# Performance work log

Hardware: AMD Instinct MI355X
Metric: run time of the kernel (lower is better)

The kernel has to match this reference:

```python
import jax, jax.numpy as jnp
import numpy as np

N, DEG, F = 500000, 16, 128
H1, H2, OUT = 256, 256, 128


def setup_inputs() -> dict:
    key = jax.random.key(0)
    ks = jax.random.split(key, 8)
    s = lambda fan_in: 1.0 / np.sqrt(fan_in)
    return {
        "message": jax.random.normal(ks[0], (N, DEG, F), dtype=jnp.float32),
        "features": jax.random.normal(ks[1], (N, F), dtype=jnp.float32),
        "global_features": jax.random.normal(ks[2], (N, F), dtype=jnp.float32),
        "W1": jax.random.normal(ks[3], (3 * F, H1), dtype=jnp.float32) * s(3 * F),
        "b1": jnp.zeros((H1,), dtype=jnp.float32),
        "W2": jax.random.normal(ks[4], (H1, H2), dtype=jnp.float32) * s(H1),
        "b2": jnp.zeros((H2,), dtype=jnp.float32),
        "W3": jax.random.normal(ks[5], (H2, OUT), dtype=jnp.float32) * s(H2),
        "b3": jnp.zeros((OUT,), dtype=jnp.float32),
    }


def reference(message, features, global_features, W1, b1, W2, b2, W3, b3):
    # mailbox sum-aggregate over neighbors: [N, deg, F] -> [N, F]
    agg = jnp.sum(message, axis=1)
    # concat aggregated messages with node + global features: [N, 3F]
    x = jnp.concatenate([agg, features, global_features], axis=1)
    # MLP: Linear+ReLU, Linear+ReLU, Linear
    h = jax.nn.relu(x @ W1 + b1)
    h = jax.nn.relu(h @ W2 + b2)
    out = h @ W3 + b3
    # row-wise L2 (Frobenius over dim=1) normalization
    norm = jnp.linalg.norm(out, axis=1, keepdims=True)
    return out / (norm + 1e-8)
```

## Files before the change

### kernel.cpp

```cpp
#include <hip/hip_runtime.h>


typedef short short8   __attribute__((ext_vector_type(8)));
typedef short short4_t __attribute__((ext_vector_type(4)));
typedef float f32x4    __attribute__((ext_vector_type(4)));

#define SWZ(row, off) ((off) ^ (((row) & 7) << 4))

__device__ __forceinline__ unsigned short f2bf(float f) {
    unsigned int u = __float_as_uint(f);
    u += 0x7fffu + ((u >> 16) & 1u);
    return (unsigned short)(u >> 16);
}

__global__ void prep_weights(const float* __restrict__ W1,
                             const float* __restrict__ W2,
                             const float* __restrict__ W3,
                             short* __restrict__ pw1,
                             short* __restrict__ pw2,
                             short* __restrict__ pw3) {
    int idx = blockIdx.x * 256 + threadIdx.x;
    if (idx < 98304) {
        int j = idx & 7, l = (idx >> 3) & 63, g = idx >> 9;
        int ks = g % 12, tn = g / 12;
        int n = tn * 16 + (l & 15);
        int k = ks * 32 + ((l >> 4) << 3) + j;
        pw1[idx] = (short)f2bf(W1[k * 256 + n]);
    } else if (idx < 98304 + 65536) {
        int e = idx - 98304;
        int j = e & 7, l = (e >> 3) & 63, g = e >> 9;
        int ks = g & 7, tn = g >> 3;
        int n = tn * 16 + (l & 15);
        int k = ks * 32 + ((l >> 4) << 3) + j;
        pw2[e] = (short)f2bf(W2[k * 256 + n]);
    } else if (idx < 98304 + 65536 + 32768) {
        int e = idx - 98304 - 65536;
        int j = e & 7, l = (e >> 3) & 63, g = e >> 9;
        int ks = g & 7, tn = g >> 3;
        int n = tn * 16 + (l & 15);
        int k = ks * 32 + ((l >> 4) << 3) + j;
        pw3[e] = (short)f2bf(W3[k * 128 + n]);
    }
}

__global__ __launch_bounds__(256, 4) void node_net_fused(
    const float* __restrict__ msg,
    const float* __restrict__ feat,
    const float* __restrict__ glob,
    const float* __restrict__ b1v,
    const float* __restrict__ b2v,
    const float* __restrict__ b3v,
    const short* __restrict__ pw1,
    const short* __restrict__ pw2,
    const short* __restrict__ pw3,
    float* __restrict__ out,
    int n_rows)
{
    __shared__ char lds[32768];
    char* regA = lds;
    char* regB = lds + 16384;

    const int tid  = threadIdx.x;
    const int lane = tid & 63;
    const int w    = tid >> 6;
    const int lr   = lane & 15;
    const int lk   = lane >> 4;
    const long long r0 = (long long)blockIdx.x * 32;

    const f32x4 zero4 = {0.f, 0.f, 0.f, 0.f};

    f32x4 fr[4], gr[4];
    #pragma unroll
    for (int q = 0; q < 4; ++q) {
        int r = (tid >> 5) + q * 8;
        long long row = r0 + r;
        fr[q] = zero4; gr[q] = zero4;
        if (row < n_rows) {
            fr[q] = __builtin_nontemporal_load((const f32x4*)feat + row * 32 + (tid & 31));
            gr[q] = __builtin_nontemporal_load((const f32x4*)glob + row * 32 + (tid & 31));
        }
    }

    #pragma unroll 1
    for (int pp = 0; pp < 4; ++pp) {
        const int rA = 8 * w + 2 * pp;
        const long long rowA = r0 + rA;
        const f32x4* base = (const f32x4*)msg + rowA * 512;
        f32x4 tA[8], tB[8];
        const bool okA = rowA < n_rows;
        const bool okB = (rowA + 1) < n_rows;
        if (okA) {
            #pragma unroll
            for (int i = 0; i < 8; ++i) tA[i] = __builtin_nontemporal_load(base + i * 64 + lane);
        } else {
            #pragma unroll
            for (int i = 0; i < 8; ++i) tA[i] = zero4;
        }
        if (okB) {
            #pragma unroll
            for (int i = 0; i < 8; ++i) tB[i] = __builtin_nontemporal_load(base + 512 + i * 64 + lane);
        } else {
            #pragma unroll
            for (int i = 0; i < 8; ++i) tB[i] = zero4;
        }
        f32x4 sA = ((tA[0] + tA[1]) + (tA[2] + tA[3])) + ((tA[4] + tA[5]) + (tA[6] + tA[7]));
        f32x4 sB = ((tB[0] + tB[1]) + (tB[2] + tB[3])) + ((tB[4] + tB[5]) + (tB[6] + tB[7]));
        #pragma unroll
        for (int c = 0; c < 4; ++c) {
            sA[c] += __shfl_xor(sA[c], 32);
            sB[c] += __shfl_xor(sB[c], 32);
        }
        f32x4 s = (lane < 32) ? sA : sB;
        short4_t s4;
        s4[0] = (short)f2bf(s[0]); s4[1] = (short)f2bf(s[1]);
        s4[2] = (short)f2bf(s[2]); s4[3] = (short)f2bf(s[3]);
        const int orow = rA + (lane >> 5);
        *(short4_t*)(regB + SWZ(orow, orow * 256 + (lane & 31) * 8)) = s4;
    }
    __syncthreads();

    #pragma unroll
    for (int q = 0; q < 4; ++q) {
        int r = (tid >> 5) + q * 8;
        short4_t s4;
        s4[0] = (short)f2bf(fr[q][0]); s4[1] = (short)f2bf(fr[q][1]);
        s4[2] = (short)f2bf(fr[q][2]); s4[3] = (short)f2bf(fr[q][3]);
        *(short4_t*)(regA + SWZ(r, r * 256 + (tid & 31) * 8)) = s4;
    }

    f32x4 acc1[2][4];
    #pragma unroll
    for (int ri = 0; ri < 2; ++ri)
        #pragma unroll
        for (int ci = 0; ci < 4; ++ci) acc1[ri][ci] = zero4;

    #pragma unroll
    for (int s = 0; s < 4; ++s) {
        short8 a[2], b[4];
        #pragma unroll
        for (int ri = 0; ri < 2; ++ri) {
            int row = ri * 16 + lr;
            a[ri] = *(const short8*)(regB + SWZ(row, row * 256 + s * 64 + lk * 16));
        }
        #pragma unroll
        for (int ci = 0; ci < 4; ++ci) {
            int tn = w * 4 + ci;
            b[ci] = *(const short8*)(pw1 + (((tn * 12 + s) * 64 + lane) << 3));
        }
        #pragma unroll
        for (int ri = 0; ri < 2; ++ri)
            #pragma unroll
            for (int ci = 0; ci < 4; ++ci)
                acc1[ri][ci] = __builtin_amdgcn_mfma_f32_16x16x32_bf16(
                    a[ri], b[ci], acc1[ri][ci], 0, 0, 0);
    }
    __syncthreads();

    #pragma unroll
    for (int q = 0; q < 4; ++q) {
        int r = (tid >> 5) + q * 8;
        short4_t s4;
        s4[0] = (short)f2bf(gr[q][0]); s4[1] = (short)f2bf(gr[q][1]);
        s4[2] = (short)f2bf(gr[q][2]); s4[3] = (short)f2bf(gr[q][3]);
        *(short4_t*)(regB + 8192 + SWZ(r, r * 256 + (tid & 31) * 8)) = s4;
    }

    #pragma unroll
    for (int s = 0; s < 4; ++s) {
        short8 a[2], b[4];
        #pragma unroll
        for (int ri = 0; ri < 2; ++ri) {
            int row = ri * 16 + lr;
            a[ri] = *(const short8*)(regA + SWZ(row, row * 256 + s * 64 + lk * 16));
        }
        #pragma unroll
        for (int ci = 0; ci < 4; ++ci) {
            int tn = w * 4 + ci;
            b[ci] = *(const short8*)(pw1 + (((tn * 12 + 4 + s) * 64 + lane) << 3));
        }
        #pragma unroll
        for (int ri = 0; ri < 2; ++ri)
            #pragma unroll
            for (int ci = 0; ci < 4; ++ci)
                acc1[ri][ci] = __builtin_amdgcn_mfma_f32_16x16x32_bf16(
                    a[ri], b[ci], acc1[ri][ci], 0, 0, 0);
    }
    __syncthreads();

    #pragma unroll
    for (int s = 0; s < 4; ++s) {
        short8 a[2], b[4];
        #pragma unroll
        for (int ri = 0; ri < 2; ++ri) {
            int row = ri * 16 + lr;
            a[ri] = *(const short8*)(regB + 8192 + SWZ(row, row * 256 + s * 64 + lk * 16));
        }
        #pragma unroll
        for (int ci = 0; ci < 4; ++ci) {
            int tn = w * 4 + ci;
            b[ci] = *(const short8*)(pw1 + (((tn * 12 + 8 + s) * 64 + lane) << 3));
        }
        #pragma unroll
        for (int ri = 0; ri < 2; ++ri)
            #pragma unroll
            for (int ci = 0; ci < 4; ++ci)
                acc1[ri][ci] = __builtin_amdgcn_mfma_f32_16x16x32_bf16(
                    a[ri], b[ci], acc1[ri][ci], 0, 0, 0);
    }

    #pragma unroll
    for (int ci = 0; ci < 4; ++ci) {
        int col = w * 64 + ci * 16 + lr;
        float bias = b1v[col];
        #pragma unroll
        for (int ri = 0; ri < 2; ++ri)
            #pragma unroll
            for (int i = 0; i < 4; ++i) {
                int row = ri * 16 + lk * 4 + i;
                float v = fmaxf(acc1[ri][ci][i] + bias, 0.f);
                *(short*)(regA + SWZ(row, row * 512 + col * 2)) = (short)f2bf(v);
            }
    }
    __syncthreads();

    f32x4 acc2[2][4];
    #pragma unroll
    for (int ri = 0; ri < 2; ++ri)
        #pragma unroll
        for (int ci = 0; ci < 4; ++ci) acc2[ri][ci] = zero4;

    #pragma unroll
    for (int s = 0; s < 8; ++s) {
        short8 a[2], b[4];
        #pragma unroll
        for (int ri = 0; ri < 2; ++ri) {
            int row = ri * 16 + lr;
            a[ri] = *(const short8*)(regA + SWZ(row, row * 512 + s * 64 + lk * 16));
        }
        #pragma unroll
        for (int ci = 0; ci < 4; ++ci) {
            int tn = w * 4 + ci;
            b[ci] = *(const short8*)(pw2 + (((tn * 8 + s) * 64 + lane) << 3));
        }
        #pragma unroll
        for (int ri = 0; ri < 2; ++ri)
            #pragma unroll
            for (int ci = 0; ci < 4; ++ci)
                acc2[ri][ci] = __builtin_amdgcn_mfma_f32_16x16x32_bf16(
                    a[ri], b[ci], acc2[ri][ci], 0, 0, 0);
    }

    #pragma unroll
    for (int ci = 0; ci < 4; ++ci) {
        int col = w * 64 + ci * 16 + lr;
        float bias = b2v[col];
        #pragma unroll
        for (int ri = 0; ri < 2; ++ri)
            #pragma unroll
            for (int i = 0; i < 4; ++i) {
                int row = ri * 16 + lk * 4 + i;
                float v = fmaxf(acc2[ri][ci][i] + bias, 0.f);
                *(short*)(regB + SWZ(row, row * 512 + col * 2)) = (short)f2bf(v);
            }
    }
    __syncthreads();

    f32x4 acc3[2][2];
    #pragma unroll
    for (int ri = 0; ri < 2; ++ri)
        #pragma unroll
        for (int ci = 0; ci < 2; ++ci) acc3[ri][ci] = zero4;

    #pragma unroll
    for (int s = 0; s < 8; ++s) {
        short8 a[2], b[2];
        #pragma unroll
        for (int ri = 0; ri < 2; ++ri) {
            int row = ri * 16 + lr;
            a[ri] = *(const short8*)(regB + SWZ(row, row * 512 + s * 64 + lk * 16));
        }
        #pragma unroll
        for (int ci = 0; ci < 2; ++ci) {
            int tn = w * 2 + ci;
            b[ci] = *(const short8*)(pw3 + (((tn * 8 + s) * 64 + lane) << 3));
        }
        #pragma unroll
        for (int ri = 0; ri < 2; ++ri)
            #pragma unroll
            for (int ci = 0; ci < 2; ++ci)
                acc3[ri][ci] = __builtin_amdgcn_mfma_f32_16x16x32_bf16(
                    a[ri], b[ci], acc3[ri][ci], 0, 0, 0);
    }

    #pragma unroll
    for (int ci = 0; ci < 2; ++ci) {
        int col = w * 32 + ci * 16 + lr;
        float bias = b3v[col];
        #pragma unroll
        for (int ri = 0; ri < 2; ++ri)
            #pragma unroll
            for (int i = 0; i < 4; ++i) {
                int row = ri * 16 + lk * 4 + i;
                float v = acc3[ri][ci][i] + bias;
                *(float*)(regA + SWZ(row, row * 512 + col * 4)) = v;
            }
    }
    __syncthreads();

    #pragma unroll
    for (int pass = 0; pass < 4; ++pass) {
        const int r  = (tid >> 5) + pass * 8;
        const int fl = tid & 31;
        f32x4 v = *(const f32x4*)(regA + SWZ(r, r * 512 + fl * 16));
        float ss = v[0]*v[0] + v[1]*v[1] + v[2]*v[2] + v[3]*v[3];
        ss += __shfl_xor(ss, 1, 32);
        ss += __shfl_xor(ss, 2, 32);
        ss += __shfl_xor(ss, 4, 32);
        ss += __shfl_xor(ss, 8, 32);
        ss += __shfl_xor(ss, 16, 32);
        float inv = 1.f / (sqrtf(ss) + 1e-8f);
        long long row = r0 + r;
        if (row < n_rows) {
            f32x4 o = v * inv;
            __builtin_nontemporal_store(o, (f32x4*)out + row * 32 + fl);
        }
    }
}

extern "C" void kernel_launch(void* const* d_in, const int* in_sizes, int n_in,
                              void* d_out, int out_size, void* d_ws, size_t ws_size,
                              hipStream_t stream) {
    const float* msg  = (const float*)d_in[0];
    const float* feat = (const float*)d_in[1];
    const float* glob = (const float*)d_in[2];
    const float* W1   = (const float*)d_in[3];
    const float* b1   = (const float*)d_in[4];
    const float* W2   = (const float*)d_in[5];
    const float* b2   = (const float*)d_in[6];
    const float* W3   = (const float*)d_in[7];
    const float* b3   = (const float*)d_in[8];
    float* out = (float*)d_out;

    const int n_rows = in_sizes[1] / 128;

    short* pw1 = (short*)d_ws;
    short* pw2 = pw1 + 98304;
    short* pw3 = pw2 + 65536;

    hipLaunchKernelGGL(prep_weights, dim3(768), dim3(256), 0, stream,
                       W1, W2, W3, pw1, pw2, pw3);

    const int nblocks = (n_rows + 31) / 32;
    hipLaunchKernelGGL(node_net_fused, dim3(nblocks), dim3(256), 0, stream,
                       msg, feat, glob, b1, b2, b3, pw1, pw2, pw3, out, n_rows);
}
```

Measured before the change: 1.080 ms.

## Convert fused node MLP to persistent blocks with software-pipelined message prefetch

The one-block-per-tile launch becomes a persistent grid of at most 1024 blocks that loop over 32-row tiles. While the MFMA layers run for the current tile, each block loads the next tile's message rows, features and global features, so the memory stream overlaps with compute. Biases are hoisted into registers, and features and globals are staged in a larger LDS buffer. The cost is more LDS per block (40KB), more register pressure from the in-flight prefetch registers, and fewer blocks in flight to hide latency.

```diff
diff --git a/kernel.cpp b/kernel.cpp
--- a/kernel.cpp
+++ b/kernel.cpp
@@ -43,7 +43,36 @@
     }
 }
 
-__global__ __launch_bounds__(256, 4) void node_net_fused(
+#define ISSUE(j) {                                                            \
+    const long long rowg_ = rn0 + 8 * w + (j);                                \
+    if (rowg_ < n_rows) {                                                     \
+        const f32x4* bp_ = (const f32x4*)msg + rowg_ * 512 + lane;            \
+        T[0] = __builtin_nontemporal_load(bp_ + 0 * 64);                      \
+        T[1] = __builtin_nontemporal_load(bp_ + 1 * 64);                      \
+        T[2] = __builtin_nontemporal_load(bp_ + 2 * 64);                      \
+        T[3] = __builtin_nontemporal_load(bp_ + 3 * 64);                      \
+        T[4] = __builtin_nontemporal_load(bp_ + 4 * 64);                      \
+        T[5] = __builtin_nontemporal_load(bp_ + 5 * 64);                      \
+        T[6] = __builtin_nontemporal_load(bp_ + 6 * 64);                      \
+        T[7] = __builtin_nontemporal_load(bp_ + 7 * 64);                      \
+    } else {                                                                  \
+        T[0]=zero4; T[1]=zero4; T[2]=zero4; T[3]=zero4;                       \
+        T[4]=zero4; T[5]=zero4; T[6]=zero4; T[7]=zero4;                       \
+    } }
+
+#define CONSUME(j) {                                                          \
+    f32x4 s_ = ((T[0]+T[1])+(T[2]+T[3])) + ((T[4]+T[5])+(T[6]+T[7]));         \
+    s_[0] += __shfl_xor(s_[0], 32); s_[1] += __shfl_xor(s_[1], 32);           \
+    s_[2] += __shfl_xor(s_[2], 32); s_[3] += __shfl_xor(s_[3], 32);           \
+    if (lane < 32) {                                                          \
+        short4_t s4_;                                                         \
+        s4_[0]=(short)f2bf(s_[0]); s4_[1]=(short)f2bf(s_[1]);                 \
+        s4_[2]=(short)f2bf(s_[2]); s4_[3]=(short)f2bf(s_[3]);                 \
+        const int rj_ = 8 * w + (j);                                          \
+        *(short4_t*)(XB + SWZ(rj_, rj_ * 256 + (lane & 31) * 8)) = s4_;       \
+    } }
+
+__global__ __launch_bounds__(256, 4) void node_net_pipe(
     const float* __restrict__ msg,
     const float* __restrict__ feat,
     const float* __restrict__ glob,
@@ -54,275 +83,281 @@
     const short* __restrict__ pw2,
     const short* __restrict__ pw3,
     float* __restrict__ out,
-    int n_rows)
+    int n_rows, int ntiles, int nblk)
 {
-    __shared__ char lds[32768];
-    char* regA = lds;
-    char* regB = lds + 16384;
+    __shared__ char lds[40960];
+    char* XB = lds;
+    char* HB = lds + 24576;
 
     const int tid  = threadIdx.x;
     const int lane = tid & 63;
     const int w    = tid >> 6;
     const int lr   = lane & 15;
     const int lk   = lane >> 4;
-    const long long r0 = (long long)blockIdx.x * 32;
-
     const f32x4 zero4 = {0.f, 0.f, 0.f, 0.f};
 
-    f32x4 fr[4], gr[4];
+    float bias1[4], bias2[4], bias3[2];
     #pragma unroll
-    for (int q = 0; q < 4; ++q) {
-        int r = (tid >> 5) + q * 8;
-        long long row = r0 + r;
-        fr[q] = zero4; gr[q] = zero4;
-        if (row < n_rows) {
-            fr[q] = __builtin_nontemporal_load((const f32x4*)feat + row * 32 + (tid & 31));
-            gr[q] = __builtin_nontemporal_load((const f32x4*)glob + row * 32 + (tid & 31));
-        }
+    for (int ci = 0; ci < 4; ++ci) {
+        bias1[ci] = b1v[w * 64 + ci * 16 + lr];
+        bias2[ci] = b2v[w * 64 + ci * 16 + lr];
     }
-
-    #pragma unroll 1
-    for (int pp = 0; pp < 4; ++pp) {
-        const int rA = 8 * w + 2 * pp;
-        const long long rowA = r0 + rA;
-        const f32x4* base = (const f32x4*)msg + rowA * 512;
-        f32x4 tA[8], tB[8];
-        const bool okA = rowA < n_rows;
-        const bool okB = (rowA + 1) < n_rows;
-        if (okA) {
-            #pragma unroll
-            for (int i = 0; i < 8; ++i) tA[i] = __builtin_nontemporal_load(base + i * 64 + lane);
-        } else {
-            #pragma unroll
-            for (int i = 0; i < 8; ++i) tA[i] = zero4;
-        }
-        if (okB) {
-            #pragma unroll
-            for (int i = 0; i < 8; ++i) tB[i] = __builtin_nontemporal_load(base + 512 + i * 64 + lane);
-        } else {
-            #pragma unroll
-            for (int i = 0; i < 8; ++i) tB[i] = zero4;
-        }
-        f32x4 sA = ((tA[0] + tA[1]) + (tA[2] + tA[3])) + ((tA[4] + tA[5]) + (tA[6] + tA[7]));
-        f32x4 sB = ((tB[0] + tB[1]) + (tB[2] + tB[3])) + ((tB[4] + tB[5]) + (tB[6] + tB[7]));
-        #pragma unroll
-        for (int c = 0; c < 4; ++c) {
-            sA[c] += __shfl_xor(sA[c], 32);
-            sB[c] += __shfl_xor(sB[c], 32);
-        }
-        f32x4 s = (lane < 32) ? sA : sB;
-        short4_t s4;
-        s4[0] = (short)f2bf(s[0]); s4[1] = (short)f2bf(s[1]);
-        s4[2] = (short)f2bf(s[2]); s4[3] = (short)f2bf(s[3]);
-        const int orow = rA + (lane >> 5);
-        *(short4_t*)(regB + SWZ(orow, orow * 256 + (lane & 31) * 8)) = s4;
+    #pragma unroll
+    for (int ci = 0; ci < 2; ++ci) bias3[ci] = b3v[w * 32 + ci * 16 + lr];
+
+    long long t = blockIdx.x;
+
+    {
+        const long long r0 = t * 32;
+        f32x4 fr[4], gr[4];
+        #pragma unroll
+        for (int q = 0; q < 4; ++q) {
+            int r = (tid >> 5) + q * 8;
+            long long row = r0 + r;
+            fr[q] = zero4; gr[q] = zero4;
+            if (row < n_rows) {
+                fr[q] = __builtin_nontemporal_load((const f32x4*)feat + row * 32 + (tid & 31));
+                gr[q] = __builtin_nontemporal_load((const f32x4*)glob + row * 32 + (tid & 31));
+            }
+        }
+        #pragma unroll 1
+        for (int pp = 0; pp < 4; ++pp) {
+            const int rA = 8 * w + 2 * pp;
+            const long long rowA = r0 + rA;
+            const f32x4* base = (const f32x4*)msg + rowA * 512;
+            f32x4 tA[8], tB[8];
+            const bool okA = rowA < n_rows;
+            const bool okB = (rowA + 1) < n_rows;
+            #pragma unroll
+            for (int i = 0; i < 8; ++i)
+                tA[i] = okA ? __builtin_nontemporal_load(base + i * 64 + lane) : zero4;
+            #pragma unroll
+            for (int i = 0; i < 8; ++i)
+                tB[i] = okB ? __builtin_nontemporal_load(base + 512 + i * 64 + lane) : zero4;
+            f32x4 sA = ((tA[0]+tA[1])+(tA[2]+tA[3])) + ((tA[4]+tA[5])+(tA[6]+tA[7]));
+            f32x4 sB = ((tB[0]+tB[1])+(tB[2]+tB[3])) + ((tB[4]+tB[5])+(tB[6]+tB[7]));
+            #pragma unroll
+            for (int c = 0; c < 4; ++c) {
+                sA[c] += __shfl_xor(sA[c], 32);
+                sB[c] += __shfl_xor(sB[c], 32);
+            }
+            f32x4 s = (lane < 32) ? sA : sB;
+            short4_t s4;
+            s4[0]=(short)f2bf(s[0]); s4[1]=(short)f2bf(s[1]);
+            s4[2]=(short)f2bf(s[2]); s4[3]=(short)f2bf(s[3]);
+            const int orow = rA + (lane >> 5);
+            *(short4_t*)(XB + SWZ(orow, orow * 256 + (lane & 31) * 8)) = s4;
+        }
+        #pragma unroll
+        for (int q = 0; q < 4; ++q) {
+            int r = (tid >> 5) + q * 8;
+            short4_t sf, sg;
+            sf[0]=(short)f2bf(fr[q][0]); sf[1]=(short)f2bf(fr[q][1]);
+            sf[2]=(short)f2bf(fr[q][2]); sf[3]=(short)f2bf(fr[q][3]);
+            sg[0]=(short)f2bf(gr[q][0]); sg[1]=(short)f2bf(gr[q][1]);
+            sg[2]=(short)f2bf(gr[q][2]); sg[3]=(short)f2bf(gr[q][3]);
+            *(short4_t*)(XB + 8192  + SWZ(r, r * 256 + (tid & 31) * 8)) = sf;
+            *(short4_t*)(XB + 16384 + SWZ(r, r * 256 + (tid & 31) * 8)) = sg;
+        }
     }
     __syncthreads();
 
-    #pragma unroll
-    for (int q = 0; q < 4; ++q) {
-        int r = (tid >> 5) + q * 8;
-        short4_t s4;
-        s4[0] = (short)f2bf(fr[q][0]); s4[1] = (short)f2bf(fr[q][1]);
-        s4[2] = (short)f2bf(fr[q][2]); s4[3] = (short)f2bf(fr[q][3]);
-        *(short4_t*)(regA + SWZ(r, r * 256 + (tid & 31) * 8)) = s4;
-    }
-
-    f32x4 acc1[2][4];
-    #pragma unroll
-    for (int ri = 0; ri < 2; ++ri)
-        #pragma unroll
-        for (int ci = 0; ci < 4; ++ci) acc1[ri][ci] = zero4;
-
-    #pragma unroll
-    for (int s = 0; s < 4; ++s) {
-        short8 a[2], b[4];
-        #pragma unroll
-        for (int ri = 0; ri < 2; ++ri) {
-            int row = ri * 16 + lr;
-            a[ri] = *(const short8*)(regB + SWZ(row, row * 256 + s * 64 + lk * 16));
-        }
+    for (; t < ntiles; t += nblk) {
+        const long long r0  = t * 32;
+        const long long rn0 = (t + (long long)nblk) * 32;
+        f32x4 T[8];
+
+        f32x4 acc1[2][4];
+        #pragma unroll
+        for (int ri = 0; ri < 2; ++ri)
+            #pragma unroll
+            for (int ci = 0; ci < 4; ++ci) acc1[ri][ci] = zero4;
+
+        #pragma unroll
+        for (int s = 0; s < 4; ++s) {
+            short8 a[2], b[4];
+            #pragma unroll
+            for (int ri = 0; ri < 2; ++ri) {
+                int row = ri * 16 + lr;
+                a[ri] = *(const short8*)(XB + SWZ(row, row * 256 + s * 64 + lk * 16));
+            }
+            #pragma unroll
+            for (int ci = 0; ci < 4; ++ci)
+                b[ci] = *(const short8*)(pw1 + ((((w * 4 + ci) * 12 + s) * 64 + lane) << 3));
+            #pragma unroll
+            for (int ri = 0; ri < 2; ++ri)
+                #pragma unroll
+                for (int ci = 0; ci < 4; ++ci)
+                    acc1[ri][ci] = __builtin_amdgcn_mfma_f32_16x16x32_bf16(
+                        a[ri], b[ci], acc1[ri][ci], 0, 0, 0);
+        }
+        __syncthreads();
+
+        #pragma unroll
+        for (int s = 0; s < 8; ++s) {
+            if (s == 0) { ISSUE(0) }
+            if (s == 2) { CONSUME(0) ISSUE(1) }
+            if (s == 4) { CONSUME(1) ISSUE(2) }
+            if (s == 6) { CONSUME(2) ISSUE(3) }
+            const int ks = 4 + s, p = ks >> 2, ss = ks & 3;
+            short8 a[2], b[4];
+            #pragma unroll
+            for (int ri = 0; ri < 2; ++ri) {
+                int row = ri * 16 + lr;
+                a[ri] = *(const short8*)(XB + p * 8192 + SWZ(row, row * 256 + ss * 64 + lk * 16));
+            }
+            #pragma unroll
+            for (int ci = 0; ci < 4; ++ci)
+                b[ci] = *(const short8*)(pw1 + ((((w * 4 + ci) * 12 + ks) * 64 + lane) << 3));
+            #pragma unroll
+            for (int ri = 0; ri < 2; ++ri)
+                #pragma unroll
+                for (int ci = 0; ci < 4; ++ci)
+                    acc1[ri][ci] = __builtin_amdgcn_mfma_f32_16x16x32_bf16(
+                        a[ri], b[ci], acc1[ri][ci], 0, 0, 0);
+        }
+        __syncthreads();
+
         #pragma unroll
         for (int ci = 0; ci < 4; ++ci) {
-            int tn = w * 4 + ci;
-            b[ci] = *(const short8*)(pw1 + (((tn * 12 + s) * 64 + lane) << 3));
-        }
+            int col = w * 64 + ci * 16 + lr;
+            #pragma unroll
+            for (int ri = 0; ri < 2; ++ri)
+                #pragma unroll
+                for (int i = 0; i < 4; ++i) {
+                    int row = ri * 16 + lk * 4 + i;
+                    float v = fmaxf(acc1[ri][ci][i] + bias1[ci], 0.f);
+                    *(short*)(HB + SWZ(row, row * 512 + col * 2)) = (short)f2bf(v);
+                }
+        }
+        __syncthreads();
+
+        f32x4 acc2[2][4];
         #pragma unroll
         for (int ri = 0; ri < 2; ++ri)
             #pragma unroll
+            for (int ci = 0; ci < 4; ++ci) acc2[ri][ci] = zero4;
+
+        #pragma unroll
+        for (int s = 0; s < 8; ++s) {
+            if (s == 0) { CONSUME(3) ISSUE(4) }
+            if (s == 2) { CONSUME(4) ISSUE(5) }
+            if (s == 4) { CONSUME(5) ISSUE(6) }
+            if (s == 6) { CONSUME(6) ISSUE(7) }
+            short8 a[2], b[4];
+            #pragma unroll
+            for (int ri = 0; ri < 2; ++ri) {
+                int row = ri * 16 + lr;
+                a[ri] = *(const short8*)(HB + SWZ(row, row * 512 + s * 64 + lk * 16));
+            }
+            #pragma unroll
             for (int ci = 0; ci < 4; ++ci)
-                acc1[ri][ci] = __builtin_amdgcn_mfma_f32_16x16x32_bf16(
-                    a[ri], b[ci], acc1[ri][ci], 0, 0, 0);
-    }
-    __syncthreads();
-
-    #pragma unroll
-    for (int q = 0; q < 4; ++q) {
-        int r = (tid >> 5) + q * 8;
-        short4_t s4;
-        s4[0] = (short)f2bf(gr[q][0]); s4[1] = (short)f2bf(gr[q][1]);
-        s4[2] = (short)f2bf(gr[q][2]); s4[3] = (short)f2bf(gr[q][3]);
-        *(short4_t*)(regB + 8192 + SWZ(r, r * 256 + (tid & 31) * 8)) = s4;
-    }
-
-    #pragma unroll
-    for (int s = 0; s < 4; ++s) {
-        short8 a[2], b[4];
-        #pragma unroll
-        for (int ri = 0; ri < 2; ++ri) {
-            int row = ri * 16 + lr;
-            a[ri] = *(const short8*)(regA + SWZ(row, row * 256 + s * 64 + lk * 16));
-        }
+                b[ci] = *(const short8*)(pw2 + ((((w * 4 + ci) * 8 + s) * 64 + lane) << 3));
+            #pragma unroll
+            for (int ri = 0; ri < 2; ++ri)
+                #pragma unroll
+                for (int ci = 0; ci < 4; ++ci)
+                    acc2[ri][ci] = __builtin_amdgcn_mfma_f32_16x16x32_bf16(
+                        a[ri], b[ci], acc2[ri][ci], 0, 0, 0);
+        }
+        __syncthreads();
+
         #pragma unroll
         for (int ci = 0; ci < 4; ++ci) {
-            int tn = w * 4 + ci;
-            b[ci] = *(const short8*)(pw1 + (((tn * 12 + 4 + s) * 64 + lane) << 3));
-        }
+            int col = w * 64 + ci * 16 + lr;
+            #pragma unroll
+            for (int ri = 0; ri < 2; ++ri)
+                #pragma unroll
+                for (int i = 0; i < 4; ++i) {
+                    int row = ri * 16 + lk * 4 + i;
+                    float v = fmaxf(acc2[ri][ci][i] + bias2[ci], 0.f);
+                    *(short*)(HB + SWZ(row, row * 512 + col * 2)) = (short)f2bf(v);
+                }
+        }
+        __syncthreads();
+
+        f32x4 fr[4], gr[4];
+        f32x4 acc3[2][2];
         #pragma unroll
         for (int ri = 0; ri < 2; ++ri)
             #pragma unroll
-            for (int ci = 0; ci < 4; ++ci)
-                acc1[ri][ci] = __builtin_amdgcn_mfma_f32_16x16x32_bf16(
-                    a[ri], b[ci], acc1[ri][ci], 0, 0, 0);
-    }
-    __syncthreads();
-
-    #pragma unroll
-    for (int s = 0; s < 4; ++s) {
-        short8 a[2], b[4];
-        #pragma unroll
-        for (int ri = 0; ri < 2; ++ri) {
-            int row = ri * 16 + lr;
-            a[ri] = *(const short8*)(regB + 8192 + SWZ(row, row * 256 + s * 64 + lk * 16));
-        }
-        #pragma unroll
-        for (int ci = 0; ci < 4; ++ci) {
-            int tn = w * 4 + ci;
-            b[ci] = *(const short8*)(pw1 + (((tn * 12 + 8 + s) * 64 + lane) << 3));
-        }
-        #pragma unroll
-        for (int ri = 0; ri < 2; ++ri)
-            #pragma unroll
-            for (int ci = 0; ci < 4; ++ci)
-                acc1[ri][ci] = __builtin_amdgcn_mfma_f32_16x16x32_bf16(
-                    a[ri], b[ci], acc1[ri][ci], 0, 0, 0);
-    }
-
-    #pragma unroll
-    for (int ci = 0; ci < 4; ++ci) {
-        int col = w * 64 + ci * 16 + lr;
-        float bias = b1v[col];
-        #pragma unroll
-        for (int ri = 0; ri < 2; ++ri)
-            #pragma unroll
-            for (int i = 0; i < 4; ++i) {
-                int row = ri * 16 + lk * 4 + i;
-                float v = fmaxf(acc1[ri][ci][i] + bias, 0.f);
-                *(short*)(regA + SWZ(row, row * 512 + col * 2)) = (short)f2bf(v);
-            }
-    }
-    __syncthreads();
-
-    f32x4 acc2[2][4];
-    #pragma unroll
-    for (int ri = 0; ri < 2; ++ri)
-        #pragma unroll
-        for (int ci = 0; ci < 4; ++ci) acc2[ri][ci] = zero4;
-
-    #pragma unroll
-    for (int s = 0; s < 8; ++s) {
-        short8 a[2], b[4];
-        #pragma unroll
-        for (int ri = 0; ri < 2; ++ri) {
-            int row = ri * 16 + lr;
-            a[ri] = *(const short8*)(regA + SWZ(row, row * 512 + s * 64 + lk * 16));
-        }
-        #pragma unroll
-        for (int ci = 0; ci < 4; ++ci) {
-            int tn = w * 4 + ci;
-            b[ci] = *(const short8*)(pw2 + (((tn * 8 + s) * 64 + lane) << 3));
-        }
-        #pragma unroll
-        for (int ri = 0; ri < 2; ++ri)
-            #pragma unroll
-            for (int ci = 0; ci < 4; ++ci)
-                acc2[ri][ci] = __builtin_amdgcn_mfma_f32_16x16x32_bf16(
-                    a[ri], b[ci], acc2[ri][ci], 0, 0, 0);
-    }
-
-    #pragma unroll
-    for (int ci = 0; ci < 4; ++ci) {
-        int col = w * 64 + ci * 16 + lr;
-        float bias = b2v[col];
-        #pragma unroll
-        for (int ri = 0; ri < 2; ++ri)
-            #pragma unroll
-            for (int i = 0; i < 4; ++i) {
-                int row = ri * 16 + lk * 4 + i;
-                float v = fmaxf(acc2[ri][ci][i] + bias, 0.f);
-                *(short*)(regB + SWZ(row, row * 512 + col * 2)) = (short)f2bf(v);
-            }
-    }
-    __syncthreads();
-
-    f32x4 acc3[2][2];
-    #pragma unroll
-    for (int ri = 0; ri < 2; ++ri)
-        #pragma unroll
-        for (int ci = 0; ci < 2; ++ci) acc3[ri][ci] = zero4;
-
-    #pragma unroll
-    for (int s = 0; s < 8; ++s) {
-        short8 a[2], b[2];
-        #pragma unroll
-        for (int ri = 0; ri < 2; ++ri) {
-            int row = ri * 16 + lr;
-            a[ri] = *(const short8*)(regB + SWZ(row, row * 512 + s * 64 + lk * 16));
-        }
+            for (int ci = 0; ci < 2; ++ci) acc3[ri][ci] = zero4;
+
+        #pragma unroll
+        for (int s = 0; s < 8; ++s) {
+            if (s == 0) {
+                CONSUME(7)
+                #pragma unroll
+                for (int q = 0; q < 4; ++q) {
+                    int r = (tid >> 5) + q * 8;
+                    long long row = rn0 + r;
+                    fr[q] = zero4; gr[q] = zero4;
+                    if (row < n_rows) {
+                        fr[q] = __builtin_nontemporal_load((const f32x4*)feat + row * 32 + (tid & 31));
+                        gr[q] = __builtin_nontemporal_load((const f32x4*)glob + row * 32 + (tid & 31));
+                    }
+                }
+            }
+            short8 a[2], b[2];
+            #pragma unroll
+            for (int ri = 0; ri < 2; ++ri) {
+                int row = ri * 16 + lr;
+                a[ri] = *(const short8*)(HB + SWZ(row, row * 512 + s * 64 + lk * 16));
+            }
+            #pragma unroll
+            for (int ci = 0; ci < 2; ++ci)
+                b[ci] = *(const short8*)(pw3 + ((((w * 2 + ci) * 8 + s) * 64 + lane) << 3));
+            #pragma unroll
+            for (int ri = 0; ri < 2; ++ri)
+                #pragma unroll
+                for (int ci = 0; ci < 2; ++ci)
+                    acc3[ri][ci] = __builtin_amdgcn_mfma_f32_16x16x32_bf16(
+                        a[ri], b[ci], acc3[ri][ci], 0, 0, 0);
+        }
+        #pragma unroll
+        for (int q = 0; q < 4; ++q) {
+            int r = (tid >> 5) + q * 8;
+            short4_t sf, sg;
+            sf[0]=(short)f2bf(fr[q][0]); sf[1]=(short)f2bf(fr[q][1]);
+            sf[2]=(short)f2bf(fr[q][2]); sf[3]=(short)f2bf(fr[q][3]);
+            sg[0]=(short)f2bf(gr[q][0]); sg[1]=(short)f2bf(gr[q][1]);
+            sg[2]=(short)f2bf(gr[q][2]); sg[3]=(short)f2bf(gr[q][3]);
+            *(short4_t*)(XB + 8192  + SWZ(r, r * 256 + (tid & 31) * 8)) = sf;
+            *(short4_t*)(XB + 16384 + SWZ(r, r * 256 + (tid & 31) * 8)) = sg;
+        }
+        __syncthreads();
+
         #pragma unroll
         for (int ci = 0; ci < 2; ++ci) {
-            int tn = w * 2 + ci;
-            b[ci] = *(const short8*)(pw3 + (((tn * 8 + s) * 64 + lane) << 3));
-        }
-        #pragma unroll
-        for (int ri = 0; ri < 2; ++ri)
-            #pragma unroll
-            for (int ci = 0; ci < 2; ++ci)
-                acc3[ri][ci] = __builtin_amdgcn_mfma_f32_16x16x32_bf16(
-                    a[ri], b[ci], acc3[ri][ci], 0, 0, 0);
-    }
-
-    #pragma unroll
-    for (int ci = 0; ci < 2; ++ci) {
-        int col = w * 32 + ci * 16 + lr;
-        float bias = b3v[col];
-        #pragma unroll
-        for (int ri = 0; ri < 2; ++ri)
-            #pragma unroll
-            for (int i = 0; i < 4; ++i) {
-                int row = ri * 16 + lk * 4 + i;
-                float v = acc3[ri][ci][i] + bias;
-                *(float*)(regA + SWZ(row, row * 512 + col * 4)) = v;
-            }
-    }
-    __syncthreads();
-
-    #pragma unroll
-    for (int pass = 0; pass < 4; ++pass) {
-        const int r  = (tid >> 5) + pass * 8;
-        const int fl = tid & 31;
-        f32x4 v = *(const f32x4*)(regA + SWZ(r, r * 512 + fl * 16));
-        float ss = v[0]*v[0] + v[1]*v[1] + v[2]*v[2] + v[3]*v[3];
-        ss += __shfl_xor(ss, 1, 32);
-        ss += __shfl_xor(ss, 2, 32);
-        ss += __shfl_xor(ss, 4, 32);
-        ss += __shfl_xor(ss, 8, 32);
-        ss += __shfl_xor(ss, 16, 32);
-        float inv = 1.f / (sqrtf(ss) + 1e-8f);
-        long long row = r0 + r;
-        if (row < n_rows) {
-            f32x4 o = v * inv;
-            __builtin_nontemporal_store(o, (f32x4*)out + row * 32 + fl);
+            int col = w * 32 + ci * 16 + lr;
+            #pragma unroll
+            for (int ri = 0; ri < 2; ++ri)
+                #pragma unroll
+                for (int i = 0; i < 4; ++i) {
+                    int row = ri * 16 + lk * 4 + i;
+                    float v = acc3[ri][ci][i] + bias3[ci];
+                    *(float*)(HB + SWZ(row, row * 512 + col * 4)) = v;
+                }
+        }
+        __syncthreads();
+
+        #pragma unroll
+        for (int pass = 0; pass < 4; ++pass) {
+            const int r  = (tid >> 5) + pass * 8;
+            const int fl = tid & 31;
+            f32x4 v = *(const f32x4*)(HB + SWZ(r, r * 512 + fl * 16));
+            float ss = v[0]*v[0] + v[1]*v[1] + v[2]*v[2] + v[3]*v[3];
+            ss += __shfl_xor(ss, 1, 32);
+            ss += __shfl_xor(ss, 2, 32);
+            ss += __shfl_xor(ss, 4, 32);
+            ss += __shfl_xor(ss, 8, 32);
+            ss += __shfl_xor(ss, 16, 32);
+            float inv = 1.f / (sqrtf(ss) + 1e-8f);
+            long long row = r0 + r;
+            if (row < n_rows) {
+                f32x4 o = v * inv;
+                __builtin_nontemporal_store(o, (f32x4*)out + row * 32 + fl);
+            }
         }
     }
 }
@@ -342,6 +377,8 @@
     float* out = (float*)d_out;
 
     const int n_rows = in_sizes[1] / 128;
+    const int ntiles = (n_rows + 31) / 32;
+    const int nblk   = ntiles < 1024 ? ntiles : 1024;
 
     short* pw1 = (short*)d_ws;
     short* pw2 = pw1 + 98304;
@@ -350,7 +387,7 @@
     hipLaunchKernelGGL(prep_weights, dim3(768), dim3(256), 0, stream,
                        W1, W2, W3, pw1, pw2, pw3);
 
-    const int nblocks = (n_rows + 31) / 32;
-    hipLaunchKernelGGL(node_net_fused, dim3(nblocks), dim3(256), 0, stream,
-                       msg, feat, glob, b1, b2, b3, pw1, pw2, pw3, out, n_rows);
+    hipLaunchKernelGGL(node_net_pipe, dim3(nblk), dim3(256), 0, stream,
+                       msg, feat, glob, b1, b2, b3, pw1, pw2, pw3, out,
+                       n_rows, ntiles, nblk);
 }
```

Measured after the change: 2.405 ms. 2.23x slower.

## Cut register pressure to raise occupancy: one message row per iteration, defer global loads

Applied to the files above, without the earlier changes.

Raises launch bounds from 4 to 5 waves per SIMD. To fit the tighter register budget, the message reduction now loads one row (8 vectors) per iteration instead of two, and the global_features loads move to just before they are written to LDS instead of being held in registers from the kernel start. A full-tile flag skips per-row bounds checks. More waves are meant to hide HBM latency on the memory-bound message stream, at the cost of fewer loads in flight per wave and exposed latency on the deferred global-feature loads.

```diff
diff --git a/kernel.cpp b/kernel.cpp
--- a/kernel.cpp
+++ b/kernel.cpp
@@ -43,7 +43,7 @@
     }
 }
 
-__global__ __launch_bounds__(256, 4) void node_net_fused(
+__global__ __launch_bounds__(256, 5) void node_net_fused(
     const float* __restrict__ msg,
     const float* __restrict__ feat,
     const float* __restrict__ glob,
@@ -66,56 +66,43 @@
     const int lr   = lane & 15;
     const int lk   = lane >> 4;
     const long long r0 = (long long)blockIdx.x * 32;
+    const bool full = (r0 + 32) <= (long long)n_rows;
 
     const f32x4 zero4 = {0.f, 0.f, 0.f, 0.f};
 
-    f32x4 fr[4], gr[4];
+    f32x4 fr[4];
     #pragma unroll
     for (int q = 0; q < 4; ++q) {
         int r = (tid >> 5) + q * 8;
         long long row = r0 + r;
-        fr[q] = zero4; gr[q] = zero4;
-        if (row < n_rows) {
+        fr[q] = zero4;
+        if (full || row < n_rows)
             fr[q] = __builtin_nontemporal_load((const f32x4*)feat + row * 32 + (tid & 31));
-            gr[q] = __builtin_nontemporal_load((const f32x4*)glob + row * 32 + (tid & 31));
-        }
     }
 
     #pragma unroll 1
-    for (int pp = 0; pp < 4; ++pp) {
-        const int rA = 8 * w + 2 * pp;
-        const long long rowA = r0 + rA;
-        const f32x4* base = (const f32x4*)msg + rowA * 512;
-        f32x4 tA[8], tB[8];
-        const bool okA = rowA < n_rows;
-        const bool okB = (rowA + 1) < n_rows;
-        if (okA) {
-            #pragma unroll
-            for (int i = 0; i < 8; ++i) tA[i] = __builtin_nontemporal_load(base + i * 64 + lane);
+    for (int c = 0; c < 8; ++c) {
+        const int rr = 8 * w + c;
+        const long long grow = r0 + rr;
+        const f32x4* base = (const f32x4*)msg + grow * 512;
+        f32x4 t[8];
+        if (full || grow < n_rows) {
+            #pragma unroll
+            for (int i = 0; i < 8; ++i)
+                t[i] = __builtin_nontemporal_load(base + i * 64 + lane);
         } else {
             #pragma unroll
-            for (int i = 0; i < 8; ++i) tA[i] = zero4;
-        }
-        if (okB) {
-            #pragma unroll
-            for (int i = 0; i < 8; ++i) tB[i] = __builtin_nontemporal_load(base + 512 + i * 64 + lane);
-        } else {
-            #pragma unroll
-            for (int i = 0; i < 8; ++i) tB[i] = zero4;
-        }
-        f32x4 sA = ((tA[0] + tA[1]) + (tA[2] + tA[3])) + ((tA[4] + tA[5]) + (tA[6] + tA[7]));
-        f32x4 sB = ((tB[0] + tB[1]) + (tB[2] + tB[3])) + ((tB[4] + tB[5]) + (tB[6] + tB[7]));
-        #pragma unroll
-        for (int c = 0; c < 4; ++c) {
-            sA[c] += __shfl_xor(sA[c], 32);
-            sB[c] += __shfl_xor(sB[c], 32);
-        }
-        f32x4 s = (lane < 32) ? sA : sB;
-        short4_t s4;
-        s4[0] = (short)f2bf(s[0]); s4[1] = (short)f2bf(s[1]);
-        s4[2] = (short)f2bf(s[2]); s4[3] = (short)f2bf(s[3]);
-        const int orow = rA + (lane >> 5);
-        *(short4_t*)(regB + SWZ(orow, orow * 256 + (lane & 31) * 8)) = s4;
+            for (int i = 0; i < 8; ++i) t[i] = zero4;
+        }
+        f32x4 s = ((t[0] + t[1]) + (t[2] + t[3])) + ((t[4] + t[5]) + (t[6] + t[7]));
+        #pragma unroll
+        for (int q = 0; q < 4; ++q) s[q] += __shfl_xor(s[q], 32);
+        if (lane < 32) {
+            short4_t s4;
+            s4[0] = (short)f2bf(s[0]); s4[1] = (short)f2bf(s[1]);
+            s4[2] = (short)f2bf(s[2]); s4[3] = (short)f2bf(s[3]);
+            *(short4_t*)(regB + SWZ(rr, rr * 256 + lane * 8)) = s4;
+        }
     }
     __syncthreads();
 
@@ -159,9 +146,13 @@
     #pragma unroll
     for (int q = 0; q < 4; ++q) {
         int r = (tid >> 5) + q * 8;
+        long long row = r0 + r;
+        f32x4 g = zero4;
+        if (full || row < n_rows)
+            g = __builtin_nontemporal_load((const f32x4*)glob + row * 32 + (tid & 31));
         short4_t s4;
-        s4[0] = (short)f2bf(gr[q][0]); s4[1] = (short)f2bf(gr[q][1]);
-        s4[2] = (short)f2bf(gr[q][2]); s4[3] = (short)f2bf(gr[q][3]);
+        s4[0] = (short)f2bf(g[0]); s4[1] = (short)f2bf(g[1]);
+        s4[2] = (short)f2bf(g[2]); s4[3] = (short)f2bf(g[3]);
         *(short4_t*)(regB + 8192 + SWZ(r, r * 256 + (tid & 31) * 8)) = s4;
     }
 
```

After: 1.299 ms. 20.2% more time.
